# Kernel optimization log

Hardware: AMD Instinct MI355X
Metric: run time of the kernel (lower is better)

Reference implementation:

```python
import jax, jax.numpy as jnp
import numpy as np

B, H, W, C = 8, 32, 32, 512
NUM_HEADS, DIM_HEAD = 16, 32


def setup_inputs() -> dict:
    key = jax.random.key(0)
    ks = jax.random.split(key, 6)
    return {
        "x": jax.random.normal(ks[0], (B, H, W, C), dtype=jnp.float32),
        "shared_rel_pos": jax.random.normal(ks[1], (NUM_HEADS, H * W, H * W), dtype=jnp.float32),
        "W_qkv": jax.random.normal(ks[2], (C, 3 * NUM_HEADS * DIM_HEAD), dtype=jnp.float32) * 0.02,
        "b_qkv": jax.random.normal(ks[3], (3 * NUM_HEADS * DIM_HEAD,), dtype=jnp.float32) * 0.02,
        "W_proj": jax.random.normal(ks[4], (NUM_HEADS * DIM_HEAD, C), dtype=jnp.float32) * 0.02,
        "b_proj": jax.random.normal(ks[5], (C,), dtype=jnp.float32) * 0.02,
    }


def reference(x, shared_rel_pos, W_qkv, b_qkv, W_proj, b_proj):
    b, h, w, c = x.shape
    n = h * w
    scale = DIM_HEAD ** -0.5
    # qkv projection; head_first layout: [B, N, heads, 3*dim_head]
    qkv = x.reshape(b, n, c) @ W_qkv + b_qkv
    qkv = qkv.reshape(b, n, NUM_HEADS, 3 * DIM_HEAD).transpose(0, 2, 1, 3)  # [B, heads, N, 3*dh]
    q, k, v = jnp.split(qkv, 3, axis=-1)  # each [B, heads, N, dh]
    attn = jnp.einsum("bhnd,bhmd->bhnm", q, k) * scale
    attn = attn + shared_rel_pos[None]  # bias shared across batch
    attn = jax.nn.softmax(attn, axis=-1)
    out = jnp.einsum("bhnm,bhmd->bhnd", attn, v)  # [B, heads, N, dh]
    out = out.transpose(0, 2, 1, 3).reshape(b, h, w, NUM_HEADS * DIM_HEAD)
    return out @ W_proj + b_proj
```

## Files before the change

### kernel.cpp

```cpp
#include <hip/hip_runtime.h>
#include <math.h>


constexpr int kB  = 8;
constexpr int kNH = 16;
constexpr int kDH = 32;
constexpr int kC  = 512;
constexpr int kN  = 1024;
constexpr int kBN = kB * kN;
constexpr int kQKV = 3 * kNH * kDH;

typedef __attribute__((ext_vector_type(8))) short bf16x8;
typedef __attribute__((ext_vector_type(4))) float f32x4;

__device__ __forceinline__ unsigned short f2bf(float f) {
    unsigned int u = __float_as_uint(f);
    unsigned int r = (u + 0x7FFFu + ((u >> 16) & 1u)) >> 16;
    return (unsigned short)r;
}

__global__ __launch_bounds__(256) void convert_x(
    const float* __restrict__ in, unsigned short* __restrict__ out)
{
    const int i = blockIdx.x * 256 + threadIdx.x;
    float4 v = reinterpret_cast<const float4*>(in)[i];
    ushort4 o;
    o.x = f2bf(v.x); o.y = f2bf(v.y); o.z = f2bf(v.z); o.w = f2bf(v.w);
    reinterpret_cast<ushort4*>(out)[i] = o;
}

__global__ __launch_bounds__(256) void transpose_convert(
    const float* __restrict__ in, unsigned short* __restrict__ out, int R, int C)
{
    __shared__ float T[64][65];
    const int tid = threadIdx.x;
    const int c0 = blockIdx.x * 64, r0 = blockIdx.y * 64;
    #pragma unroll
    for (int p = 0; p < 4; p++) {
        const int r = (tid >> 4) + p * 16, c = (tid & 15) * 4;
        float4 v = *reinterpret_cast<const float4*>(in + (size_t)(r0 + r) * C + c0 + c);
        T[r][c + 0] = v.x; T[r][c + 1] = v.y; T[r][c + 2] = v.z; T[r][c + 3] = v.w;
    }
    __syncthreads();
    #pragma unroll
    for (int p = 0; p < 4; p++) {
        const int c = (tid >> 4) + p * 16, r4 = (tid & 15) * 4;
        ushort4 w;
        w.x = f2bf(T[r4 + 0][c]); w.y = f2bf(T[r4 + 1][c]);
        w.z = f2bf(T[r4 + 2][c]); w.w = f2bf(T[r4 + 3][c]);
        *reinterpret_cast<ushort4*>(out + (size_t)(c0 + c) * R + r0 + r4) = w;
    }
}

__global__ __launch_bounds__(256) void qkv_mfma(
    const unsigned short* __restrict__ A,
    const unsigned short* __restrict__ Bt,
    const float* __restrict__ bias,
    unsigned short* __restrict__ q_ws,
    unsigned short* __restrict__ k_ws,
    unsigned short* __restrict__ v_ws)
{
    __shared__ unsigned short As[128 * 72];
    __shared__ unsigned short Bs[128 * 72];
    const int tid = threadIdx.x;
    const int wave = tid >> 6, lane = tid & 63;
    const int col = lane & 15, hi = lane >> 4;
    const int wr = wave >> 1, wc = wave & 1;
    const int m0 = blockIdx.x * 128, n0 = blockIdx.y * 128;

    f32x4 acc[4][4] = {};
    for (int k0 = 0; k0 < kC; k0 += 64) {
        #pragma unroll
        for (int i = 0; i < 4; i++) {
            const int ch = i * 256 + tid, row = ch >> 3, cc = (ch & 7) * 8;
            *reinterpret_cast<bf16x8*>(&As[row * 72 + cc]) =
                *reinterpret_cast<const bf16x8*>(A + (size_t)(m0 + row) * kC + k0 + cc);
            *reinterpret_cast<bf16x8*>(&Bs[row * 72 + cc]) =
                *reinterpret_cast<const bf16x8*>(Bt + (size_t)(n0 + row) * kC + k0 + cc);
        }
        __syncthreads();
        #pragma unroll
        for (int kk = 0; kk < 2; kk++) {
            bf16x8 af[4], bfr[4];
            #pragma unroll
            for (int mt = 0; mt < 4; mt++)
                af[mt] = *reinterpret_cast<const bf16x8*>(
                    &As[(wr * 64 + mt * 16 + col) * 72 + kk * 32 + 8 * hi]);
            #pragma unroll
            for (int nt = 0; nt < 4; nt++)
                bfr[nt] = *reinterpret_cast<const bf16x8*>(
                    &Bs[(wc * 64 + nt * 16 + col) * 72 + kk * 32 + 8 * hi]);
            #pragma unroll
            for (int mt = 0; mt < 4; mt++)
                #pragma unroll
                for (int nt = 0; nt < 4; nt++)
                    acc[mt][nt] = __builtin_amdgcn_mfma_f32_16x16x32_bf16(
                        af[mt], bfr[nt], acc[mt][nt], 0, 0, 0);
        }
        __syncthreads();
    }

    const float scale = 0.17677669529663687f;
    #pragma unroll
    for (int nt = 0; nt < 4; nt++) {
        const int n = n0 + wc * 64 + nt * 16 + col;
        const int head = n / 96;
        const int r = n - head * 96;
        const float bv = bias[n];
        #pragma unroll
        for (int mt = 0; mt < 4; mt++)
            #pragma unroll
            for (int reg = 0; reg < 4; reg++) {
                const int m = m0 + wr * 64 + mt * 16 + 4 * hi + reg;
                const int bb = m >> 10, np = m & 1023;
                const float v = acc[mt][nt][reg] + bv;
                const size_t base = ((size_t)(bb * kNH + head) * kN + np) * kDH;
                if (r < 32)      q_ws[base + r]      = f2bf(v * scale);
                else if (r < 64) k_ws[base + r - 32] = f2bf(v);
                else             v_ws[base + r - 64] = f2bf(v);
            }
    }
}

__global__ __launch_bounds__(256) void attn_kernel(
    const unsigned short* __restrict__ q_ws,
    const unsigned short* __restrict__ k_ws,
    const unsigned short* __restrict__ v_ws,
    const float* __restrict__ rel,
    unsigned short* __restrict__ aout)
{
    __shared__ unsigned short Ks[64 * 72];
    __shared__ unsigned short Vt[32 * 72];
    __shared__ unsigned short Pl[4][16 * 72];

    const int tid  = threadIdx.x;
    const int wave = tid >> 6;
    const int lane = tid & 63;
    const int col  = lane & 15;
    const int hi   = lane >> 4;
    const int h = blockIdx.y >> 3;
    const int b = blockIdx.y & 7;
    const int bh = b * kNH + h;
    const int r0 = blockIdx.x * 64 + wave * 16;

    const bf16x8 q_frag = *reinterpret_cast<const bf16x8*>(
        q_ws + ((size_t)bh * kN + r0 + col) * kDH + 8 * hi);

    const unsigned short* kb = k_ws + (size_t)bh * kN * kDH;
    const unsigned short* vb = v_ws + (size_t)bh * kN * kDH;
    const float* relb = rel + ((size_t)h * kN + r0) * kN + col;

    f32x4 o0 = {0.f, 0.f, 0.f, 0.f};
    f32x4 o1 = {0.f, 0.f, 0.f, 0.f};
    float mrun[4] = {-1e30f, -1e30f, -1e30f, -1e30f};
    float lrun[4] = {0.f, 0.f, 0.f, 0.f};

    const int srow = tid >> 2;
    const int sd0  = (tid & 3) * 8;

    for (int c0 = 0; c0 < kN; c0 += 64) {
        {
            bf16x8 kv = *reinterpret_cast<const bf16x8*>(kb + (size_t)(c0 + srow) * kDH + sd0);
            *reinterpret_cast<bf16x8*>(&Ks[srow * 72 + sd0]) = kv;
            bf16x8 vv = *reinterpret_cast<const bf16x8*>(vb + (size_t)(c0 + srow) * kDH + sd0);
            #pragma unroll
            for (int j = 0; j < 8; j++)
                Vt[(sd0 + j) * 72 + srow] = (unsigned short)vv[j];
        }
        __syncthreads();

        f32x4 s[4];
        #pragma unroll
        for (int t = 0; t < 4; t++) {
            const bf16x8 kf = *reinterpret_cast<const bf16x8*>(&Ks[(t * 16 + col) * 72 + 8 * hi]);
            const f32x4 z = {0.f, 0.f, 0.f, 0.f};
            s[t] = __builtin_amdgcn_mfma_f32_16x16x32_bf16(q_frag, kf, z, 0, 0, 0);
        }

        #pragma unroll
        for (int t = 0; t < 4; t++)
            #pragma unroll
            for (int reg = 0; reg < 4; reg++)
                s[t][reg] += relb[(size_t)(4 * hi + reg) * kN + c0 + t * 16];

        float cm[4], nm[4], corr[4], psum[4];
        #pragma unroll
        for (int reg = 0; reg < 4; reg++) {
            cm[reg] = fmaxf(fmaxf(s[0][reg], s[1][reg]), fmaxf(s[2][reg], s[3][reg]));
            #pragma unroll
            for (int off = 1; off < 16; off <<= 1)
                cm[reg] = fmaxf(cm[reg], __shfl_xor(cm[reg], off));
            nm[reg] = fmaxf(mrun[reg], cm[reg]);
            corr[reg] = __expf(mrun[reg] - nm[reg]);
            mrun[reg] = nm[reg];
            psum[reg] = 0.f;
        }
        #pragma unroll
        for (int t = 0; t < 4; t++)
            #pragma unroll
            for (int reg = 0; reg < 4; reg++) {
                s[t][reg] = __expf(s[t][reg] - nm[reg]);
                psum[reg] += s[t][reg];
            }
        #pragma unroll
        for (int reg = 0; reg < 4; reg++) {
            #pragma unroll
            for (int off = 1; off < 16; off <<= 1)
                psum[reg] += __shfl_xor(psum[reg], off);
            lrun[reg] = lrun[reg] * corr[reg] + psum[reg];
            o0[reg] *= corr[reg];
            o1[reg] *= corr[reg];
        }

        unsigned short* pw = &Pl[wave][0];
        #pragma unroll
        for (int t = 0; t < 4; t++)
            #pragma unroll
            for (int reg = 0; reg < 4; reg++)
                pw[(4 * hi + reg) * 72 + t * 16 + col] = f2bf(s[t][reg]);

        #pragma unroll
        for (int half = 0; half < 2; half++) {
            const bf16x8 pa = *reinterpret_cast<const bf16x8*>(
                &Pl[wave][col * 72 + half * 32 + 8 * hi]);
            const bf16x8 v0 = *reinterpret_cast<const bf16x8*>(
                &Vt[(0 * 16 + col) * 72 + half * 32 + 8 * hi]);
            const bf16x8 v1 = *reinterpret_cast<const bf16x8*>(
                &Vt[(1 * 16 + col) * 72 + half * 32 + 8 * hi]);
            o0 = __builtin_amdgcn_mfma_f32_16x16x32_bf16(pa, v0, o0, 0, 0, 0);
            o1 = __builtin_amdgcn_mfma_f32_16x16x32_bf16(pa, v1, o1, 0, 0, 0);
        }
        __syncthreads();
    }

    #pragma unroll
    for (int reg = 0; reg < 4; reg++) {
        const float inv = 1.0f / lrun[reg];
        unsigned short* orow = aout + ((size_t)b * kN + r0 + 4 * hi + reg) * kC + h * kDH;
        orow[col]      = f2bf(o0[reg] * inv);
        orow[16 + col] = f2bf(o1[reg] * inv);
    }
}

__global__ __launch_bounds__(256) void proj_mfma(
    const unsigned short* __restrict__ A,
    const unsigned short* __restrict__ Bt,
    const float* __restrict__ bias,
    float* __restrict__ out)
{
    __shared__ unsigned short As[128 * 72];
    __shared__ unsigned short Bs[128 * 72];
    const int tid = threadIdx.x;
    const int wave = tid >> 6, lane = tid & 63;
    const int col = lane & 15, hi = lane >> 4;
    const int wr = wave >> 1, wc = wave & 1;
    const int m0 = blockIdx.x * 128, n0 = blockIdx.y * 128;

    f32x4 acc[4][4] = {};
    for (int k0 = 0; k0 < kC; k0 += 64) {
        #pragma unroll
        for (int i = 0; i < 4; i++) {
            const int ch = i * 256 + tid, row = ch >> 3, cc = (ch & 7) * 8;
            *reinterpret_cast<bf16x8*>(&As[row * 72 + cc]) =
                *reinterpret_cast<const bf16x8*>(A + (size_t)(m0 + row) * kC + k0 + cc);
            *reinterpret_cast<bf16x8*>(&Bs[row * 72 + cc]) =
                *reinterpret_cast<const bf16x8*>(Bt + (size_t)(n0 + row) * kC + k0 + cc);
        }
        __syncthreads();
        #pragma unroll
        for (int kk = 0; kk < 2; kk++) {
            bf16x8 af[4], bfr[4];
            #pragma unroll
            for (int mt = 0; mt < 4; mt++)
                af[mt] = *reinterpret_cast<const bf16x8*>(
                    &As[(wr * 64 + mt * 16 + col) * 72 + kk * 32 + 8 * hi]);
            #pragma unroll
            for (int nt = 0; nt < 4; nt++)
                bfr[nt] = *reinterpret_cast<const bf16x8*>(
                    &Bs[(wc * 64 + nt * 16 + col) * 72 + kk * 32 + 8 * hi]);
            #pragma unroll
            for (int mt = 0; mt < 4; mt++)
                #pragma unroll
                for (int nt = 0; nt < 4; nt++)
                    acc[mt][nt] = __builtin_amdgcn_mfma_f32_16x16x32_bf16(
                        af[mt], bfr[nt], acc[mt][nt], 0, 0, 0);
        }
        __syncthreads();
    }

    #pragma unroll
    for (int nt = 0; nt < 4; nt++) {
        const int n = n0 + wc * 64 + nt * 16 + col;
        const float bv = bias[n];
        #pragma unroll
        for (int mt = 0; mt < 4; mt++)
            #pragma unroll
            for (int reg = 0; reg < 4; reg++) {
                const int m = m0 + wr * 64 + mt * 16 + 4 * hi + reg;
                out[(size_t)m * kC + n] = acc[mt][nt][reg] + bv;
            }
    }
}

extern "C" void kernel_launch(void* const* d_in, const int* in_sizes, int n_in,
                              void* d_out, int out_size, void* d_ws, size_t ws_size,
                              hipStream_t stream) {
    const float* x     = (const float*)d_in[0];
    const float* rel   = (const float*)d_in[1];
    const float* Wqkv  = (const float*)d_in[2];
    const float* bqkv  = (const float*)d_in[3];
    const float* Wproj = (const float*)d_in[4];
    const float* bproj = (const float*)d_in[5];
    float* out = (float*)d_out;

    unsigned short* ws = (unsigned short*)d_ws;
    const size_t qkv_elems = (size_t)kB * kNH * kN * kDH;
    unsigned short* q_ws = ws;                    ws += qkv_elems;
    unsigned short* k_ws = ws;                    ws += qkv_elems;
    unsigned short* v_ws = ws;                    ws += qkv_elems;
    unsigned short* a_ws = ws;                    ws += (size_t)kBN * kC;
    unsigned short* xb   = ws;                    ws += (size_t)kBN * kC;
    unsigned short* Wqt  = ws;                    ws += (size_t)kQKV * kC;
    unsigned short* Wpt  = ws;                    ws += (size_t)kC * kC;

    convert_x<<<dim3(kBN * kC / 4 / 256), 256, 0, stream>>>(x, xb);
    transpose_convert<<<dim3(kQKV / 64, kC / 64), 256, 0, stream>>>(Wqkv, Wqt, kC, kQKV);
    transpose_convert<<<dim3(kC / 64, kC / 64), 256, 0, stream>>>(Wproj, Wpt, kC, kC);

    qkv_mfma<<<dim3(kBN / 128, kQKV / 128), 256, 0, stream>>>(xb, Wqt, bqkv, q_ws, k_ws, v_ws);
    attn_kernel<<<dim3(kN / 64, kB * kNH), 256, 0, stream>>>(q_ws, k_ws, v_ws, rel, a_ws);
    proj_mfma<<<dim3(kBN / 128, kC / 128), 256, 0, stream>>>(a_ws, Wpt, bproj, out);
}
```

Baseline: 262.7 us.

## Transpose S tile, store V pre-transposed, prefetch K/V, use exp2 softmax

The QKV epilogue now writes V in a [bh, d, n] layout and folds log2(e) into the q scale. The attention kernel swaps the MFMA operands so each lane holds one query row's scores, which lets it read rel_pos with vector f32x4 loads. Row max and sum reductions drop to two cross-lane shuffles, and exp2 replaces expf. K and V tiles are prefetched into registers one iteration ahead, and the scattered per-element V transpose into LDS is removed. The costs are extra shuffles to move the correction and normalisation factors back into the output layout, and the V global stores in the QKV kernel become strided.

Measured after the change: 237.5 us. 9.6% less time.

```diff
diff --git a/kernel.cpp b/kernel.cpp
--- a/kernel.cpp
+++ b/kernel.cpp
@@ -13,10 +13,20 @@
 typedef __attribute__((ext_vector_type(8))) short bf16x8;
 typedef __attribute__((ext_vector_type(4))) float f32x4;
 
+#define LOG2E 1.4426950408889634f
+
 __device__ __forceinline__ unsigned short f2bf(float f) {
     unsigned int u = __float_as_uint(f);
     unsigned int r = (u + 0x7FFFu + ((u >> 16) & 1u)) >> 16;
     return (unsigned short)r;
+}
+
+__device__ __forceinline__ float exp2_fast(float x) {
+#if __has_builtin(__builtin_amdgcn_exp2f)
+    return __builtin_amdgcn_exp2f(x);
+#else
+    return exp2f(x);
+#endif
 }
 
 __global__ __launch_bounds__(256) void convert_x(
@@ -100,7 +110,7 @@
         __syncthreads();
     }
 
-    const float scale = 0.17677669529663687f;
+    const float scale = 0.25503238645263514f;
     #pragma unroll
     for (int nt = 0; nt < 4; nt++) {
         const int n = n0 + wc * 64 + nt * 16 + col;
@@ -114,10 +124,13 @@
                 const int m = m0 + wr * 64 + mt * 16 + 4 * hi + reg;
                 const int bb = m >> 10, np = m & 1023;
                 const float v = acc[mt][nt][reg] + bv;
-                const size_t base = ((size_t)(bb * kNH + head) * kN + np) * kDH;
-                if (r < 32)      q_ws[base + r]      = f2bf(v * scale);
-                else if (r < 64) k_ws[base + r - 32] = f2bf(v);
-                else             v_ws[base + r - 64] = f2bf(v);
+                const size_t bh = (size_t)(bb * kNH + head);
+                if (r < 32)
+                    q_ws[(bh * kN + np) * kDH + r] = f2bf(v * scale);
+                else if (r < 64)
+                    k_ws[(bh * kN + np) * kDH + r - 32] = f2bf(v);
+                else
+                    v_ws[(bh * kDH + (r - 64)) * kN + np] = f2bf(v);
             }
     }
 }
@@ -133,100 +146,104 @@
     __shared__ unsigned short Vt[32 * 72];
     __shared__ unsigned short Pl[4][16 * 72];
 
-    const int tid  = threadIdx.x;
-    const int wave = tid >> 6;
-    const int lane = tid & 63;
-    const int col  = lane & 15;
-    const int hi   = lane >> 4;
-    const int h = blockIdx.y >> 3;
-    const int b = blockIdx.y & 7;
+    const int tid = threadIdx.x;
+    const int wave = tid >> 6, lane = tid & 63;
+    const int col = lane & 15, hi = lane >> 4;
+    const int h = blockIdx.y >> 3, b = blockIdx.y & 7;
     const int bh = b * kNH + h;
     const int r0 = blockIdx.x * 64 + wave * 16;
 
     const bf16x8 q_frag = *reinterpret_cast<const bf16x8*>(
         q_ws + ((size_t)bh * kN + r0 + col) * kDH + 8 * hi);
 
-    const unsigned short* kb = k_ws + (size_t)bh * kN * kDH;
-    const unsigned short* vb = v_ws + (size_t)bh * kN * kDH;
-    const float* relb = rel + ((size_t)h * kN + r0) * kN + col;
+    const unsigned short* kb  = k_ws + (size_t)bh * kN * kDH;
+    const unsigned short* vtb = v_ws + (size_t)bh * kDH * kN;
+    const float* relq = rel + ((size_t)h * kN + r0 + col) * kN;
 
     f32x4 o0 = {0.f, 0.f, 0.f, 0.f};
     f32x4 o1 = {0.f, 0.f, 0.f, 0.f};
-    float mrun[4] = {-1e30f, -1e30f, -1e30f, -1e30f};
-    float lrun[4] = {0.f, 0.f, 0.f, 0.f};
-
-    const int srow = tid >> 2;
-    const int sd0  = (tid & 3) * 8;
+    float m2 = -1e30f, l = 0.f;
+
+    const int kr = tid >> 2, kd8 = (tid & 3) * 8;
+    const int vr = tid >> 3, vk8 = (tid & 7) * 8;
+
+    bf16x8 kreg = *reinterpret_cast<const bf16x8*>(kb + (size_t)kr * kDH + kd8);
+    bf16x8 vreg = *reinterpret_cast<const bf16x8*>(vtb + (size_t)vr * kN + vk8);
 
     for (int c0 = 0; c0 < kN; c0 += 64) {
-        {
-            bf16x8 kv = *reinterpret_cast<const bf16x8*>(kb + (size_t)(c0 + srow) * kDH + sd0);
-            *reinterpret_cast<bf16x8*>(&Ks[srow * 72 + sd0]) = kv;
-            bf16x8 vv = *reinterpret_cast<const bf16x8*>(vb + (size_t)(c0 + srow) * kDH + sd0);
-            #pragma unroll
-            for (int j = 0; j < 8; j++)
-                Vt[(sd0 + j) * 72 + srow] = (unsigned short)vv[j];
-        }
-        __syncthreads();
+        *reinterpret_cast<bf16x8*>(&Ks[kr * 72 + kd8]) = kreg;
+        *reinterpret_cast<bf16x8*>(&Vt[vr * 72 + vk8]) = vreg;
+        __syncthreads();
+        if (c0 + 64 < kN) {
+            kreg = *reinterpret_cast<const bf16x8*>(kb + (size_t)(c0 + 64 + kr) * kDH + kd8);
+            vreg = *reinterpret_cast<const bf16x8*>(vtb + (size_t)vr * kN + c0 + 64 + vk8);
+        }
 
         f32x4 s[4];
         #pragma unroll
         for (int t = 0; t < 4; t++) {
-            const bf16x8 kf = *reinterpret_cast<const bf16x8*>(&Ks[(t * 16 + col) * 72 + 8 * hi]);
+            const bf16x8 kf = *reinterpret_cast<const bf16x8*>(
+                &Ks[(t * 16 + col) * 72 + 8 * hi]);
             const f32x4 z = {0.f, 0.f, 0.f, 0.f};
-            s[t] = __builtin_amdgcn_mfma_f32_16x16x32_bf16(q_frag, kf, z, 0, 0, 0);
-        }
-
+            s[t] = __builtin_amdgcn_mfma_f32_16x16x32_bf16(kf, q_frag, z, 0, 0, 0);
+        }
+
+        #pragma unroll
+        for (int t = 0; t < 4; t++) {
+            const f32x4 b4 = *reinterpret_cast<const f32x4*>(relq + c0 + t * 16 + 4 * hi);
+            #pragma unroll
+            for (int r = 0; r < 4; r++)
+                s[t][r] = fmaf(b4[r], LOG2E, s[t][r]);
+        }
+
+        float cm = s[0][0];
         #pragma unroll
         for (int t = 0; t < 4; t++)
             #pragma unroll
-            for (int reg = 0; reg < 4; reg++)
-                s[t][reg] += relb[(size_t)(4 * hi + reg) * kN + c0 + t * 16];
-
-        float cm[4], nm[4], corr[4], psum[4];
-        #pragma unroll
-        for (int reg = 0; reg < 4; reg++) {
-            cm[reg] = fmaxf(fmaxf(s[0][reg], s[1][reg]), fmaxf(s[2][reg], s[3][reg]));
-            #pragma unroll
-            for (int off = 1; off < 16; off <<= 1)
-                cm[reg] = fmaxf(cm[reg], __shfl_xor(cm[reg], off));
-            nm[reg] = fmaxf(mrun[reg], cm[reg]);
-            corr[reg] = __expf(mrun[reg] - nm[reg]);
-            mrun[reg] = nm[reg];
-            psum[reg] = 0.f;
-        }
+            for (int r = 0; r < 4; r++)
+                cm = fmaxf(cm, s[t][r]);
+        cm = fmaxf(cm, __shfl_xor(cm, 16));
+        cm = fmaxf(cm, __shfl_xor(cm, 32));
+        const float nm = fmaxf(m2, cm);
+        const float corr = exp2_fast(m2 - nm);
+        m2 = nm;
+
+        float ps = 0.f;
         #pragma unroll
         for (int t = 0; t < 4; t++)
             #pragma unroll
-            for (int reg = 0; reg < 4; reg++) {
-                s[t][reg] = __expf(s[t][reg] - nm[reg]);
-                psum[reg] += s[t][reg];
+            for (int r = 0; r < 4; r++) {
+                s[t][r] = exp2_fast(s[t][r] - nm);
+                ps += s[t][r];
             }
-        #pragma unroll
-        for (int reg = 0; reg < 4; reg++) {
-            #pragma unroll
-            for (int off = 1; off < 16; off <<= 1)
-                psum[reg] += __shfl_xor(psum[reg], off);
-            lrun[reg] = lrun[reg] * corr[reg] + psum[reg];
-            o0[reg] *= corr[reg];
-            o1[reg] *= corr[reg];
-        }
-
-        unsigned short* pw = &Pl[wave][0];
-        #pragma unroll
-        for (int t = 0; t < 4; t++)
-            #pragma unroll
-            for (int reg = 0; reg < 4; reg++)
-                pw[(4 * hi + reg) * 72 + t * 16 + col] = f2bf(s[t][reg]);
+        ps += __shfl_xor(ps, 16);
+        ps += __shfl_xor(ps, 32);
+        l = l * corr + ps;
+
+        #pragma unroll
+        for (int r = 0; r < 4; r++) {
+            const float cq = __shfl(corr, 4 * hi + r);
+            o0[r] *= cq;
+            o1[r] *= cq;
+        }
+
+        unsigned short* pw = &Pl[wave][col * 72];
+        #pragma unroll
+        for (int t = 0; t < 4; t++) {
+            ushort4 pk;
+            pk.x = f2bf(s[t][0]); pk.y = f2bf(s[t][1]);
+            pk.z = f2bf(s[t][2]); pk.w = f2bf(s[t][3]);
+            *reinterpret_cast<ushort4*>(pw + t * 16 + 4 * hi) = pk;
+        }
 
         #pragma unroll
         for (int half = 0; half < 2; half++) {
             const bf16x8 pa = *reinterpret_cast<const bf16x8*>(
                 &Pl[wave][col * 72 + half * 32 + 8 * hi]);
             const bf16x8 v0 = *reinterpret_cast<const bf16x8*>(
-                &Vt[(0 * 16 + col) * 72 + half * 32 + 8 * hi]);
+                &Vt[col * 72 + half * 32 + 8 * hi]);
             const bf16x8 v1 = *reinterpret_cast<const bf16x8*>(
-                &Vt[(1 * 16 + col) * 72 + half * 32 + 8 * hi]);
+                &Vt[(16 + col) * 72 + half * 32 + 8 * hi]);
             o0 = __builtin_amdgcn_mfma_f32_16x16x32_bf16(pa, v0, o0, 0, 0, 0);
             o1 = __builtin_amdgcn_mfma_f32_16x16x32_bf16(pa, v1, o1, 0, 0, 0);
         }
@@ -234,11 +251,11 @@
     }
 
     #pragma unroll
-    for (int reg = 0; reg < 4; reg++) {
-        const float inv = 1.0f / lrun[reg];
-        unsigned short* orow = aout + ((size_t)b * kN + r0 + 4 * hi + reg) * kC + h * kDH;
-        orow[col]      = f2bf(o0[reg] * inv);
-        orow[16 + col] = f2bf(o1[reg] * inv);
+    for (int r = 0; r < 4; r++) {
+        const float inv = 1.0f / __shfl(l, 4 * hi + r);
+        unsigned short* orow = aout + ((size_t)b * kN + r0 + 4 * hi + r) * kC + h * kDH;
+        orow[col]      = f2bf(o0[r] * inv);
+        orow[16 + col] = f2bf(o1[r] * inv);
     }
 }
 
```
